# Kernel tuning notes

Measured on AMD Instinct MI355X. Metric: run time of the kernel, lower is better.

The kernel has to match this reference:

```python
import jax, jax.numpy as jnp
import numpy as np

NUM_HEADS = 16
HEAD_DIM = 256
FFN_HIDDEN = 512
NUM_USER_HEADS = 8
EPS = 1e-6
BATCH = 8192


def _make_mask(num_heads, head_dim, num_user_heads):
    m = np.ones((num_heads, head_dim), dtype=np.float32)
    sub = head_dim // num_heads
    m[:num_user_heads, num_user_heads * sub:] = 0.0
    return jnp.asarray(m)


def setup_inputs() -> dict:
    key = jax.random.key(0)
    ks = jax.random.split(key, 6)
    x = jax.random.normal(ks[0], (BATCH, NUM_HEADS, HEAD_DIM), dtype=jnp.float32)
    norm1_w = jnp.ones((HEAD_DIM,), dtype=jnp.float32)
    norm2_w = jnp.ones((HEAD_DIM,), dtype=jnp.float32)
    s_in = 1.0 / np.sqrt(HEAD_DIM)
    s_hid = 1.0 / np.sqrt(FFN_HIDDEN)
    w1 = jax.random.normal(ks[1], (NUM_HEADS, HEAD_DIM, FFN_HIDDEN), dtype=jnp.float32) * s_in
    w3 = jax.random.normal(ks[2], (NUM_HEADS, HEAD_DIM, FFN_HIDDEN), dtype=jnp.float32) * s_in
    w2 = jax.random.normal(ks[3], (NUM_HEADS, FFN_HIDDEN, HEAD_DIM), dtype=jnp.float32) * s_hid
    mask = _make_mask(NUM_HEADS, HEAD_DIM, NUM_USER_HEADS)
    return {"x": x, "norm1_w": norm1_w, "norm2_w": norm2_w,
            "w1": w1, "w3": w3, "w2": w2, "mask": mask}


def _rmsnorm(x, w):
    # x: (B,N,D), w: (D,)
    rms = jax.lax.rsqrt(jnp.mean(x * x, axis=-1, keepdims=True) + EPS)
    return x * rms * w


def _head_mixing(x):
    # Parameter-free cross-head sub-dim exchange:
    # mixed[:, i, j*sub:(j+1)*sub] = x[:, j, i*sub:(i+1)*sub]
    B, N, D = x.shape
    sub = D // N
    return x.reshape(B, N, N, sub).transpose(0, 2, 1, 3).reshape(B, N, D)


def reference(x, norm1_w, norm2_w, w1, w3, w2, mask):
    # UI-decoupled HeadMixing: mask zeroes item-head info flowing into user heads
    mixed = _head_mixing(_rmsnorm(x, norm1_w)) * mask[None, :, :]
    p = mixed + x
    # per-head SwiGLU FFN
    h = _rmsnorm(p, norm2_w)
    a = jnp.einsum('bnd,ndh->bnh', h, w1)  # gate
    b = jnp.einsum('bnd,ndh->bnh', h, w3)  # value
    ffn = jnp.einsum('bnh,nhd->bnd', jax.nn.silu(a) * b, w2)
    return ffn + p
```

## Files before the change

kernel.cpp:

```cpp
#include <hip/hip_runtime.h>
#include <hip/hip_bf16.h>
#include <cstdint>

#define B_SZ 8192
#define NH 16
#define HD 256
#define FH 512
#define BR 64

typedef __bf16 bf16x8 __attribute__((ext_vector_type(8)));
typedef float f32x4 __attribute__((ext_vector_type(4)));

#define VMCNT(n) asm volatile("s_waitcnt vmcnt(" #n ")" ::: "memory")
#define LGKM0()  asm volatile("s_waitcnt lgkmcnt(0)" ::: "memory")
#define MEMFENCE() asm volatile("" ::: "memory")

__device__ __forceinline__ void lds_load16(const void* g, void* l) {
  __builtin_amdgcn_global_load_lds(
      (const __attribute__((address_space(1))) unsigned char*)g,
      (__attribute__((address_space(3))) unsigned char*)l, 16, 0, 0);
}

__global__ __launch_bounds__(256) void wcvt_kernel(const float* __restrict__ w1,
                                                   const float* __restrict__ w3,
                                                   const float* __restrict__ w2,
                                                   __bf16* __restrict__ w1t,
                                                   __bf16* __restrict__ w3t,
                                                   __bf16* __restrict__ w2t) {
  int bid = blockIdx.x;
  const float* src;
  __bf16* dst;
  int K, N;
  if (bid < 2048)      { src = w1; dst = w1t; K = 256; N = 512; }
  else if (bid < 4096) { src = w3; dst = w3t; K = 256; N = 512; bid -= 2048; }
  else                 { src = w2; dst = w2t; K = 512; N = 256; bid -= 4096; }
  const int tiles_n = N >> 5, tiles_k = K >> 5;
  const int per_head = tiles_n * tiles_k;
  const int head = bid / per_head;
  const int rem = bid - head * per_head;
  const int tk = rem / tiles_n;
  const int tn = rem - tk * tiles_n;
  __shared__ float tile[32][33];
  const float* s = src + ((size_t)head * K + tk * 32) * N + tn * 32;
  const int r = threadIdx.x >> 3;
  const int c4 = (threadIdx.x & 7) * 4;
  float4 v = *(const float4*)(s + (size_t)r * N + c4);
  tile[r][c4 + 0] = v.x; tile[r][c4 + 1] = v.y;
  tile[r][c4 + 2] = v.z; tile[r][c4 + 3] = v.w;
  __syncthreads();
  __bf16 o[4] __attribute__((aligned(8)));
  #pragma unroll
  for (int j = 0; j < 4; ++j) o[j] = (__bf16)tile[c4 + j][r];
  __bf16* d = dst + ((size_t)head * N + tn * 32 + r) * K + tk * 32 + c4;
  *(uint2*)d = *(uint2*)o;
}

#define PREP_R 8
__global__ __launch_bounds__(256) void prep_kernel(const float* __restrict__ x,
                                                   const float* __restrict__ n1w,
                                                   const float* __restrict__ n2w,
                                                   const float* __restrict__ mask,
                                                   __bf16* __restrict__ p_ws,
                                                   __bf16* __restrict__ h_ws) {
  const int t = threadIdx.x;
  const int g = t >> 4;
  const int li = t & 15;
  __shared__ float xs[16 * 260];
  __shared__ float rms1s[16];

  float n1c[16], n2c[16], mc[16];
  #pragma unroll
  for (int j = 0; j < 4; ++j) {
    *(float4*)(n1c + j * 4) = *(const float4*)(n1w + g * 16 + j * 4);
    *(float4*)(n2c + j * 4) = *(const float4*)(n2w + li * 16 + j * 4);
    *(float4*)(mc + j * 4)  = *(const float4*)(mask + g * HD + li * 16 + j * 4);
  }

  for (int r = 0; r < PREP_R; ++r) {
    const int b = blockIdx.x * PREP_R + r;
    const float* xb = x + (size_t)b * (NH * HD);
    if (r) __syncthreads();

    float xv[16];
    float ss = 0.f;
    #pragma unroll
    for (int j = 0; j < 4; ++j) {
      float4 v = *(const float4*)(xb + g * HD + li * 16 + j * 4);
      *(float4*)(xs + g * 260 + li * 16 + j * 4) = v;
      xv[j * 4 + 0] = v.x; xv[j * 4 + 1] = v.y;
      xv[j * 4 + 2] = v.z; xv[j * 4 + 3] = v.w;
      ss += v.x * v.x + v.y * v.y + v.z * v.z + v.w * v.w;
    }
    #pragma unroll
    for (int d = 1; d < 16; d <<= 1) ss += __shfl_xor(ss, d);
    if (li == 0) rms1s[g] = rsqrtf(ss * (1.f / 256.f) + 1e-6f);
    __syncthreads();

    const float r1 = rms1s[li];
    float pv[16];
    float ss2 = 0.f;
    #pragma unroll
    for (int j = 0; j < 4; ++j) {
      float4 sv = *(const float4*)(xs + li * 260 + g * 16 + j * 4);
      float s4[4] = {sv.x, sv.y, sv.z, sv.w};
      #pragma unroll
      for (int q = 0; q < 4; ++q) {
        const int k = j * 4 + q;
        const float mixed = s4[q] * r1 * n1c[k] * mc[k];
        const float p = mixed + xv[k];
        pv[k] = p;
        ss2 += p * p;
      }
    }
    #pragma unroll
    for (int d = 1; d < 16; d <<= 1) ss2 += __shfl_xor(ss2, d);
    const float r2 = rsqrtf(ss2 * (1.f / 256.f) + 1e-6f);

    __bf16 pb[16] __attribute__((aligned(16)));
    __bf16 hv[16] __attribute__((aligned(16)));
    #pragma unroll
    for (int k = 0; k < 16; ++k) {
      pb[k] = (__bf16)pv[k];
      hv[k] = (__bf16)(pv[k] * r2 * n2c[k]);
    }
    __bf16* pp = p_ws + ((size_t)g * B_SZ + b) * HD + li * 16;
    *(uint4*)(pp + 0) = *(uint4*)(pb + 0);
    *(uint4*)(pp + 8) = *(uint4*)(pb + 8);
    __bf16* hp = h_ws + ((size_t)g * B_SZ + b) * HD + li * 16;
    *(uint4*)(hp + 0) = *(uint4*)(hv + 0);
    *(uint4*)(hp + 8) = *(uint4*)(hv + 8);
  }
}

__global__ __launch_bounds__(256, 2) void ffn_kernel(const __bf16* __restrict__ h_ws,
                                                     const __bf16* __restrict__ w1t,
                                                     const __bf16* __restrict__ w3t,
                                                     const __bf16* __restrict__ w2t,
                                                     const __bf16* __restrict__ p_ws,
                                                     float* __restrict__ out) {
  const int bid = blockIdx.x;
  const int head = bid & 15;
  const int stripe = bid >> 4;
  const int r0 = stripe * BR;
  const int t = threadIdx.x;
  const int wv = t >> 6, lane = t & 63;
  const int mlane = lane & 15, quad = lane >> 4;

  __shared__ __bf16 __attribute__((aligned(16))) Hs[BR * HD];
  __shared__ __bf16 __attribute__((aligned(16))) Wbuf[16384];
  __shared__ __bf16 __attribute__((aligned(16))) Sc[BR * 64];

  const __bf16* W1h = w1t + (size_t)head * FH * HD;
  const __bf16* W3h = w3t + (size_t)head * FH * HD;
  const __bf16* W2h = w2t + (size_t)head * HD * FH;

  auto stage1_issue = [&](__bf16* Ws, int hc, int kk) {
    const int rl = lane >> 3, c = lane & 7, gch = c ^ rl;
    #pragma unroll
    for (int i = 0; i < 2; ++i) {
      const int rb = wv * 16 + i * 8;
      const size_t go = (size_t)(hc * 64 + rb + rl) * HD + kk * 64 + gch * 8;
      lds_load16(W1h + go, Ws + rb * 64);
      lds_load16(W3h + go, Ws + 4096 + rb * 64);
    }
  };
  auto stage2_issue = [&](__bf16* Ws, int hc, int ks) {
    const int rl = lane >> 2, c = lane & 3, gch = c ^ (rl & 3);
    #pragma unroll
    for (int i = 0; i < 4; ++i) {
      const int rb = wv * 64 + i * 16;
      lds_load16(W2h + (size_t)(rb + rl) * FH + hc * 64 + ks * 32 + gch * 8,
                 Ws + (i >> 1) * 4096 + wv * 1024 + (i & 1) * 512);
    }
  };

  const __bf16* Hb = h_ws + ((size_t)head * B_SZ + r0) * HD;
  {
    const int rloc = lane >> 5;
    const int ch = lane & 31;
    #pragma unroll
    for (int i = 0; i < 8; ++i) {
      const int row = wv * 16 + i * 2 + rloc;
      const int gch = ch ^ (row & 15);
      lds_load16(Hb + (size_t)row * HD + gch * 8, Hs + (wv * 16 + i * 2) * HD);
    }
  }
  MEMFENCE();
  stage1_issue(Wbuf, 0, 0);
  stage1_issue(Wbuf + 8192, 0, 1);
  VMCNT(8);
  __builtin_amdgcn_s_barrier();

  f32x4 oacc[4][4];
  #pragma unroll
  for (int mt = 0; mt < 4; ++mt)
    #pragma unroll
    for (int nt = 0; nt < 4; ++nt) oacc[mt][nt] = (f32x4){0.f, 0.f, 0.f, 0.f};

  for (int hc = 0; hc < 8; ++hc) {
    f32x4 g[4], v[4];
    #pragma unroll
    for (int nt = 0; nt < 4; ++nt) {
      g[nt] = (f32x4){0.f, 0.f, 0.f, 0.f};
      v[nt] = (f32x4){0.f, 0.f, 0.f, 0.f};
    }
    #pragma unroll
    for (int kk = 0; kk < 4; ++kk) {
      __bf16* Ws = Wbuf + (kk & 1) * 8192;
      VMCNT(4);
      #pragma unroll
      for (int ks = 0; ks < 2; ++ks) {
        const int ar = wv * 16 + mlane;
        const int ach = (ks * 4 + quad) ^ (ar & 7);
        bf16x8 a1 = *(const bf16x8*)(Ws + ar * 64 + ach * 8);
        bf16x8 a3 = *(const bf16x8*)(Ws + 4096 + ar * 64 + ach * 8);
        const int gk = kk * 8 + ks * 4 + quad;
        bf16x8 b[4];
        #pragma unroll
        for (int nt = 0; nt < 4; ++nt) {
          const int row = nt * 16 + mlane;
          b[nt] = *(const bf16x8*)(Hs + row * HD + (gk ^ (row & 15)) * 8);
        }
        if (ks == 1) {
          LGKM0();
          if (kk < 2) stage1_issue(Ws, hc, kk + 2);
          else        stage2_issue(Ws, hc, kk - 2);
        }
        __builtin_amdgcn_s_setprio(1);
        #pragma unroll
        for (int nt = 0; nt < 4; ++nt) {
          g[nt] = __builtin_amdgcn_mfma_f32_16x16x32_bf16(a1, b[nt], g[nt], 0, 0, 0);
          v[nt] = __builtin_amdgcn_mfma_f32_16x16x32_bf16(a3, b[nt], v[nt], 0, 0, 0);
        }
        __builtin_amdgcn_s_setprio(0);
      }
    }

    #pragma unroll
    for (int nt = 0; nt < 4; ++nt) {
      const int row = nt * 16 + mlane;
      __bf16 sv[4] __attribute__((aligned(8)));
      #pragma unroll
      for (int r = 0; r < 4; ++r) {
        const float gg = g[nt][r];
        sv[r] = (__bf16)(gg / (1.f + __expf(-gg)) * v[nt][r]);
      }
      const int boff = wv * 32 + quad * 8;
      const int ph = ((boff >> 4) ^ (row & 7));
      char* dst = (char*)Sc + row * 128 + ph * 16 + (boff & 15);
      *(uint2*)dst = *(uint2*)sv;
    }
    LGKM0();
    __builtin_amdgcn_s_barrier();

    const int hcn = (hc + 1) & 7;
    #pragma unroll
    for (int ks = 0; ks < 2; ++ks) {
      __bf16* Ws = Wbuf + (ks & 1) * 8192;
      VMCNT(4);
      bf16x8 a2[4], b2[4];
      #pragma unroll
      for (int mt = 0; mt < 4; ++mt)
        a2[mt] = *(const bf16x8*)(Ws + (mt >> 1) * 4096 + wv * 1024 + (mt & 1) * 512
                                  + mlane * 32 + ((quad ^ (mlane & 3))) * 8);
      #pragma unroll
      for (int nt = 0; nt < 4; ++nt) {
        const int row = nt * 16 + mlane;
        b2[nt] = *(const bf16x8*)(Sc + row * 64 + (((ks * 4 + quad) ^ (row & 7))) * 8);
      }
      LGKM0();
      stage1_issue(Ws, hcn, ks);
      if (ks == 1) __builtin_amdgcn_s_barrier();
      __builtin_amdgcn_s_setprio(1);
      #pragma unroll
      for (int mt = 0; mt < 4; ++mt)
        #pragma unroll
        for (int nt = 0; nt < 4; ++nt)
          oacc[mt][nt] = __builtin_amdgcn_mfma_f32_16x16x32_bf16(a2[mt], b2[nt], oacc[mt][nt], 0, 0, 0);
      __builtin_amdgcn_s_setprio(0);
    }
  }

  VMCNT(0);

  const __bf16* Pb = p_ws + ((size_t)head * B_SZ + r0) * HD;
  float* Ob = out + (size_t)r0 * (NH * HD) + head * HD;
  #pragma unroll
  for (int mt = 0; mt < 4; ++mt)
    #pragma unroll
    for (int nt = 0; nt < 4; ++nt) {
      const int row = nt * 16 + mlane;
      const int oc = wv * 64 + mt * 16 + quad * 4;
      __bf16 pv[4] __attribute__((aligned(8)));
      *(uint2*)pv = *(const uint2*)(Pb + (size_t)row * HD + oc);
      float4 o;
      o.x = oacc[mt][nt][0] + (float)pv[0];
      o.y = oacc[mt][nt][1] + (float)pv[1];
      o.z = oacc[mt][nt][2] + (float)pv[2];
      o.w = oacc[mt][nt][3] + (float)pv[3];
      *(float4*)(Ob + (size_t)row * (NH * HD) + oc) = o;
    }
}

extern "C" void kernel_launch(void* const* d_in, const int* in_sizes, int n_in,
                              void* d_out, int out_size, void* d_ws, size_t ws_size,
                              hipStream_t stream) {
  const float* x    = (const float*)d_in[0];
  const float* n1w  = (const float*)d_in[1];
  const float* n2w  = (const float*)d_in[2];
  const float* w1   = (const float*)d_in[3];
  const float* w3   = (const float*)d_in[4];
  const float* w2   = (const float*)d_in[5];
  const float* mask = (const float*)d_in[6];
  float* out = (float*)d_out;

  char* ws = (char*)d_ws;
  __bf16* p_ws = (__bf16*)(ws + 0);
  __bf16* h_ws = (__bf16*)(ws + 67108864);
  __bf16* w1t  = (__bf16*)(ws + 134217728);
  __bf16* w3t  = (__bf16*)(ws + 138412032);
  __bf16* w2t  = (__bf16*)(ws + 142606336);

  wcvt_kernel<<<6144, 256, 0, stream>>>(w1, w3, w2, w1t, w3t, w2t);
  prep_kernel<<<1024, 256, 0, stream>>>(x, n1w, n2w, mask, p_ws, h_ws);
  ffn_kernel<<<2048, 256, 0, stream>>>(h_ws, w1t, w3t, w2t, p_ws, out);
}
```

Measured before the change: 432.9 us.

## Read FFN weights directly from global memory instead of LDS double-buffering

Removes the LDS weight staging buffer and its async global-to-LDS pipeline. W1/W3/W2 fragments are now loaded straight from global memory (relying on L2/cache) into MFMA operands. This cuts LDS use so more blocks fit per CU, and launch bounds are raised to 4 waves-per-EU to match. The prep kernel now processes fewer rows per block and launches twice as many blocks. The risk is exposed global-load latency with no prefetch overlap, plus uncoalesced weight reads.

```diff
diff --git a/kernel.cpp b/kernel.cpp
--- a/kernel.cpp
+++ b/kernel.cpp
@@ -11,9 +11,8 @@
 typedef __bf16 bf16x8 __attribute__((ext_vector_type(8)));
 typedef float f32x4 __attribute__((ext_vector_type(4)));
 
-#define VMCNT(n) asm volatile("s_waitcnt vmcnt(" #n ")" ::: "memory")
+#define VMCNT0() asm volatile("s_waitcnt vmcnt(0)" ::: "memory")
 #define LGKM0()  asm volatile("s_waitcnt lgkmcnt(0)" ::: "memory")
-#define MEMFENCE() asm volatile("" ::: "memory")
 
 __device__ __forceinline__ void lds_load16(const void* g, void* l) {
   __builtin_amdgcn_global_load_lds(
@@ -55,7 +54,7 @@
   *(uint2*)d = *(uint2*)o;
 }
 
-#define PREP_R 8
+#define PREP_R 4
 __global__ __launch_bounds__(256) void prep_kernel(const float* __restrict__ x,
                                                    const float* __restrict__ n1w,
                                                    const float* __restrict__ n2w,
@@ -132,7 +131,7 @@
   }
 }
 
-__global__ __launch_bounds__(256, 2) void ffn_kernel(const __bf16* __restrict__ h_ws,
+__global__ __launch_bounds__(256, 4) void ffn_kernel(const __bf16* __restrict__ h_ws,
                                                      const __bf16* __restrict__ w1t,
                                                      const __bf16* __restrict__ w3t,
                                                      const __bf16* __restrict__ w2t,
@@ -147,32 +146,11 @@
   const int mlane = lane & 15, quad = lane >> 4;
 
   __shared__ __bf16 __attribute__((aligned(16))) Hs[BR * HD];
-  __shared__ __bf16 __attribute__((aligned(16))) Wbuf[16384];
   __shared__ __bf16 __attribute__((aligned(16))) Sc[BR * 64];
 
   const __bf16* W1h = w1t + (size_t)head * FH * HD;
   const __bf16* W3h = w3t + (size_t)head * FH * HD;
   const __bf16* W2h = w2t + (size_t)head * HD * FH;
-
-  auto stage1_issue = [&](__bf16* Ws, int hc, int kk) {
-    const int rl = lane >> 3, c = lane & 7, gch = c ^ rl;
-    #pragma unroll
-    for (int i = 0; i < 2; ++i) {
-      const int rb = wv * 16 + i * 8;
-      const size_t go = (size_t)(hc * 64 + rb + rl) * HD + kk * 64 + gch * 8;
-      lds_load16(W1h + go, Ws + rb * 64);
-      lds_load16(W3h + go, Ws + 4096 + rb * 64);
-    }
-  };
-  auto stage2_issue = [&](__bf16* Ws, int hc, int ks) {
-    const int rl = lane >> 2, c = lane & 3, gch = c ^ (rl & 3);
-    #pragma unroll
-    for (int i = 0; i < 4; ++i) {
-      const int rb = wv * 64 + i * 16;
-      lds_load16(W2h + (size_t)(rb + rl) * FH + hc * 64 + ks * 32 + gch * 8,
-                 Ws + (i >> 1) * 4096 + wv * 1024 + (i & 1) * 512);
-    }
-  };
 
   const __bf16* Hb = h_ws + ((size_t)head * B_SZ + r0) * HD;
   {
@@ -185,10 +163,7 @@
       lds_load16(Hb + (size_t)row * HD + gch * 8, Hs + (wv * 16 + i * 2) * HD);
     }
   }
-  MEMFENCE();
-  stage1_issue(Wbuf, 0, 0);
-  stage1_issue(Wbuf + 8192, 0, 1);
-  VMCNT(8);
+  VMCNT0();
   __builtin_amdgcn_s_barrier();
 
   f32x4 oacc[4][4];
@@ -204,27 +179,20 @@
       g[nt] = (f32x4){0.f, 0.f, 0.f, 0.f};
       v[nt] = (f32x4){0.f, 0.f, 0.f, 0.f};
     }
+    const int ar = hc * 64 + wv * 16 + mlane;
     #pragma unroll
     for (int kk = 0; kk < 4; ++kk) {
-      __bf16* Ws = Wbuf + (kk & 1) * 8192;
-      VMCNT(4);
       #pragma unroll
       for (int ks = 0; ks < 2; ++ks) {
-        const int ar = wv * 16 + mlane;
-        const int ach = (ks * 4 + quad) ^ (ar & 7);
-        bf16x8 a1 = *(const bf16x8*)(Ws + ar * 64 + ach * 8);
-        bf16x8 a3 = *(const bf16x8*)(Ws + 4096 + ar * 64 + ach * 8);
+        const int koff = kk * 64 + (ks * 4 + quad) * 8;
+        bf16x8 a1 = *(const bf16x8*)(W1h + (size_t)ar * HD + koff);
+        bf16x8 a3 = *(const bf16x8*)(W3h + (size_t)ar * HD + koff);
         const int gk = kk * 8 + ks * 4 + quad;
         bf16x8 b[4];
         #pragma unroll
         for (int nt = 0; nt < 4; ++nt) {
           const int row = nt * 16 + mlane;
           b[nt] = *(const bf16x8*)(Hs + row * HD + (gk ^ (row & 15)) * 8);
-        }
-        if (ks == 1) {
-          LGKM0();
-          if (kk < 2) stage1_issue(Ws, hc, kk + 2);
-          else        stage2_issue(Ws, hc, kk - 2);
         }
         __builtin_amdgcn_s_setprio(1);
         #pragma unroll
@@ -253,24 +221,19 @@
     LGKM0();
     __builtin_amdgcn_s_barrier();
 
-    const int hcn = (hc + 1) & 7;
     #pragma unroll
     for (int ks = 0; ks < 2; ++ks) {
-      __bf16* Ws = Wbuf + (ks & 1) * 8192;
-      VMCNT(4);
       bf16x8 a2[4], b2[4];
       #pragma unroll
-      for (int mt = 0; mt < 4; ++mt)
-        a2[mt] = *(const bf16x8*)(Ws + (mt >> 1) * 4096 + wv * 1024 + (mt & 1) * 512
-                                  + mlane * 32 + ((quad ^ (mlane & 3))) * 8);
+      for (int mt = 0; mt < 4; ++mt) {
+        const int orow = wv * 64 + mt * 16 + mlane;
+        a2[mt] = *(const bf16x8*)(W2h + (size_t)orow * FH + hc * 64 + ks * 32 + quad * 8);
+      }
       #pragma unroll
       for (int nt = 0; nt < 4; ++nt) {
         const int row = nt * 16 + mlane;
         b2[nt] = *(const bf16x8*)(Sc + row * 64 + (((ks * 4 + quad) ^ (row & 7))) * 8);
       }
-      LGKM0();
-      stage1_issue(Ws, hcn, ks);
-      if (ks == 1) __builtin_amdgcn_s_barrier();
       __builtin_amdgcn_s_setprio(1);
       #pragma unroll
       for (int mt = 0; mt < 4; ++mt)
@@ -279,9 +242,8 @@
           oacc[mt][nt] = __builtin_amdgcn_mfma_f32_16x16x32_bf16(a2[mt], b2[nt], oacc[mt][nt], 0, 0, 0);
       __builtin_amdgcn_s_setprio(0);
     }
-  }
-
-  VMCNT(0);
+    __builtin_amdgcn_s_barrier();
+  }
 
   const __bf16* Pb = p_ws + ((size_t)head * B_SZ + r0) * HD;
   float* Ob = out + (size_t)r0 * (NH * HD) + head * HD;
@@ -322,6 +284,6 @@
   __bf16* w2t  = (__bf16*)(ws + 142606336);
 
   wcvt_kernel<<<6144, 256, 0, stream>>>(w1, w3, w2, w1t, w3t, w2t);
-  prep_kernel<<<1024, 256, 0, stream>>>(x, n1w, n2w, mask, p_ws, h_ws);
+  prep_kernel<<<2048, 256, 0, stream>>>(x, n1w, n2w, mask, p_ws, h_ws);
   ffn_kernel<<<2048, 256, 0, stream>>>(h_ws, w1t, w3t, w2t, p_ws, out);
 }
```

New measurement: 612.6 us. 1.42x slower.

## Rewrite prep kernel as one wavefront per row with shuffle-based head mixing

Applied to the files above, without the earlier changes.

The prep kernel no longer stages each batch row in LDS and loops over 8 rows per block with barriers. It now assigns one wavefront per batch row and four lanes per head. The head-mixing transpose is done by reloading the needed source slices straight from global memory (served by cache), with the per-head rms broadcast via shuffles. This removes LDS traffic and __syncthreads, at the cost of roughly double the global reads of x and 64 floats of registers per thread. Grid size doubles to match the 4 rows per block.

```diff
diff --git a/kernel.cpp b/kernel.cpp
--- a/kernel.cpp
+++ b/kernel.cpp
@@ -55,7 +55,6 @@
   *(uint2*)d = *(uint2*)o;
 }
 
-#define PREP_R 8
 __global__ __launch_bounds__(256) void prep_kernel(const float* __restrict__ x,
                                                    const float* __restrict__ n1w,
                                                    const float* __restrict__ n2w,
@@ -63,72 +62,72 @@
                                                    __bf16* __restrict__ p_ws,
                                                    __bf16* __restrict__ h_ws) {
   const int t = threadIdx.x;
-  const int g = t >> 4;
-  const int li = t & 15;
-  __shared__ float xs[16 * 260];
-  __shared__ float rms1s[16];
-
-  float n1c[16], n2c[16], mc[16];
-  #pragma unroll
-  for (int j = 0; j < 4; ++j) {
-    *(float4*)(n1c + j * 4) = *(const float4*)(n1w + g * 16 + j * 4);
-    *(float4*)(n2c + j * 4) = *(const float4*)(n2w + li * 16 + j * 4);
-    *(float4*)(mc + j * 4)  = *(const float4*)(mask + g * HD + li * 16 + j * 4);
-  }
-
-  for (int r = 0; r < PREP_R; ++r) {
-    const int b = blockIdx.x * PREP_R + r;
-    const float* xb = x + (size_t)b * (NH * HD);
-    if (r) __syncthreads();
-
-    float xv[16];
-    float ss = 0.f;
-    #pragma unroll
-    for (int j = 0; j < 4; ++j) {
-      float4 v = *(const float4*)(xb + g * HD + li * 16 + j * 4);
-      *(float4*)(xs + g * 260 + li * 16 + j * 4) = v;
-      xv[j * 4 + 0] = v.x; xv[j * 4 + 1] = v.y;
-      xv[j * 4 + 2] = v.z; xv[j * 4 + 3] = v.w;
-      ss += v.x * v.x + v.y * v.y + v.z * v.z + v.w * v.w;
-    }
-    #pragma unroll
-    for (int d = 1; d < 16; d <<= 1) ss += __shfl_xor(ss, d);
-    if (li == 0) rms1s[g] = rsqrtf(ss * (1.f / 256.f) + 1e-6f);
-    __syncthreads();
-
-    const float r1 = rms1s[li];
-    float pv[16];
-    float ss2 = 0.f;
-    #pragma unroll
-    for (int j = 0; j < 4; ++j) {
-      float4 sv = *(const float4*)(xs + li * 260 + g * 16 + j * 4);
-      float s4[4] = {sv.x, sv.y, sv.z, sv.w};
-      #pragma unroll
-      for (int q = 0; q < 4; ++q) {
-        const int k = j * 4 + q;
-        const float mixed = s4[q] * r1 * n1c[k] * mc[k];
-        const float p = mixed + xv[k];
-        pv[k] = p;
-        ss2 += p * p;
-      }
-    }
-    #pragma unroll
-    for (int d = 1; d < 16; d <<= 1) ss2 += __shfl_xor(ss2, d);
-    const float r2 = rsqrtf(ss2 * (1.f / 256.f) + 1e-6f);
-
+  const int wv = t >> 6, l = t & 63;
+  const int b = blockIdx.x * 4 + wv;
+  const int i = l >> 2;
+  const int c = l & 3;
+  const float* xb = x + (size_t)b * (NH * HD);
+
+  float a[64];
+  float ss = 0.f;
+  #pragma unroll
+  for (int q = 0; q < 16; ++q) {
+    float4 v = *(const float4*)(xb + i * HD + c * 64 + q * 4);
+    a[q * 4 + 0] = v.x; a[q * 4 + 1] = v.y;
+    a[q * 4 + 2] = v.z; a[q * 4 + 3] = v.w;
+    ss += v.x * v.x + v.y * v.y + v.z * v.z + v.w * v.w;
+  }
+  ss += __shfl_xor(ss, 1);
+  ss += __shfl_xor(ss, 2);
+  const float r1own = rsqrtf(ss * (1.f / 256.f) + 1e-6f);
+
+  float n1c[16];
+  #pragma unroll
+  for (int q = 0; q < 4; ++q)
+    *(float4*)(n1c + q * 4) = *(const float4*)(n1w + i * 16 + q * 4);
+
+  float ss2 = 0.f;
+  #pragma unroll
+  for (int jj = 0; jj < 4; ++jj) {
+    const int j = c * 4 + jj;
+    const float r1j = __shfl(r1own, j * 4);
+    float xsrc[16], mk[16];
+    #pragma unroll
+    for (int q = 0; q < 4; ++q) {
+      *(float4*)(xsrc + q * 4) = *(const float4*)(xb + j * HD + i * 16 + q * 4);
+      *(float4*)(mk + q * 4)   = *(const float4*)(mask + i * HD + j * 16 + q * 4);
+    }
+    #pragma unroll
+    for (int k = 0; k < 16; ++k) {
+      const float p = xsrc[k] * r1j * n1c[k] * mk[k] + a[jj * 16 + k];
+      a[jj * 16 + k] = p;
+      ss2 += p * p;
+    }
+  }
+  ss2 += __shfl_xor(ss2, 1);
+  ss2 += __shfl_xor(ss2, 2);
+  const float r2 = rsqrtf(ss2 * (1.f / 256.f) + 1e-6f);
+
+  __bf16* pp = p_ws + ((size_t)i * B_SZ + b) * HD + c * 64;
+  __bf16* hp = h_ws + ((size_t)i * B_SZ + b) * HD + c * 64;
+  #pragma unroll
+  for (int jj = 0; jj < 4; ++jj) {
+    float n2c[16];
+    #pragma unroll
+    for (int q = 0; q < 4; ++q)
+      *(float4*)(n2c + q * 4) = *(const float4*)(n2w + (c * 4 + jj) * 16 + q * 4);
     __bf16 pb[16] __attribute__((aligned(16)));
     __bf16 hv[16] __attribute__((aligned(16)));
     #pragma unroll
     for (int k = 0; k < 16; ++k) {
-      pb[k] = (__bf16)pv[k];
-      hv[k] = (__bf16)(pv[k] * r2 * n2c[k]);
-    }
-    __bf16* pp = p_ws + ((size_t)g * B_SZ + b) * HD + li * 16;
-    *(uint4*)(pp + 0) = *(uint4*)(pb + 0);
-    *(uint4*)(pp + 8) = *(uint4*)(pb + 8);
-    __bf16* hp = h_ws + ((size_t)g * B_SZ + b) * HD + li * 16;
-    *(uint4*)(hp + 0) = *(uint4*)(hv + 0);
-    *(uint4*)(hp + 8) = *(uint4*)(hv + 8);
+      const float p = a[jj * 16 + k];
+      pb[k] = (__bf16)p;
+      hv[k] = (__bf16)(p * r2 * n2c[k]);
+    }
+    *(uint4*)(pp + jj * 16 + 0) = *(uint4*)(pb + 0);
+    *(uint4*)(pp + jj * 16 + 8) = *(uint4*)(pb + 8);
+    *(uint4*)(hp + jj * 16 + 0) = *(uint4*)(hv + 0);
+    *(uint4*)(hp + jj * 16 + 8) = *(uint4*)(hv + 8);
   }
 }
 
@@ -322,6 +321,6 @@
   __bf16* w2t  = (__bf16*)(ws + 142606336);
 
   wcvt_kernel<<<6144, 256, 0, stream>>>(w1, w3, w2, w1t, w3t, w2t);
-  prep_kernel<<<1024, 256, 0, stream>>>(x, n1w, n2w, mask, p_ws, h_ws);
+  prep_kernel<<<2048, 256, 0, stream>>>(x, n1w, n2w, mask, p_ws, h_ws);
   ffn_kernel<<<2048, 256, 0, stream>>>(h_ws, w1t, w3t, w2t, p_ws, out);
 }
```

New measurement: 558.7 us. +29.1%, slower.
